# Performance work log

Hardware: AMD Instinct MI355X
Metric: run time of the kernel (lower is better)

## Reference

```python
import jax, jax.numpy as jnp
import numpy as np

BLOCKS, LAYERS, KS = 4, 2, 2
DILATIONS = [2 ** i for _ in range(BLOCKS) for i in range(LAYERS)]  # [1,2]*4
B, C_IN, N, T = 16, 2, 2048, 12
RC, DC, SC, EC, OUT = 32, 32, 256, 512, 12
L = BLOCKS * LAYERS
BN_EPS = 1e-5


def setup_inputs() -> dict:
    key = jax.random.key(0)
    ks = jax.random.split(key, 24)
    # raw inputs
    x = jax.random.normal(ks[0], (B, C_IN, N, T), dtype=jnp.float32)
    # two fixed supports: row-normalized random adjacency (dense, as in GraphWaveNet transition matrices)
    A_raw = jax.random.uniform(ks[1], (2, N, N), dtype=jnp.float32)
    A = A_raw / jnp.sum(A_raw, axis=2, keepdims=True)
    nodevec1 = jax.random.normal(ks[2], (N, 10), dtype=jnp.float32)
    nodevec2 = jax.random.normal(ks[3], (10, N), dtype=jnp.float32)
    s = 0.1  # weight scale to keep activations in a sane range
    filter_w = jax.random.normal(ks[4], (L, DC, RC, KS), dtype=jnp.float32) * s
    filter_b = jax.random.normal(ks[5], (L, DC), dtype=jnp.float32) * s
    gate_w = jax.random.normal(ks[6], (L, DC, RC, KS), dtype=jnp.float32) * s
    gate_b = jax.random.normal(ks[7], (L, DC), dtype=jnp.float32) * s
    skip_w = jax.random.normal(ks[8], (L, SC, DC), dtype=jnp.float32) * s
    skip_b = jax.random.normal(ks[9], (L, SC), dtype=jnp.float32) * s
    gcn_w = jax.random.normal(ks[10], (L, RC, 7 * DC), dtype=jnp.float32) * s
    gcn_b = jax.random.normal(ks[11], (L, RC), dtype=jnp.float32) * s
    bn_gamma = 1.0 + 0.1 * jax.random.normal(ks[12], (L, RC), dtype=jnp.float32)
    bn_beta = 0.1 * jax.random.normal(ks[13], (L, RC), dtype=jnp.float32)
    bn_mean = 0.1 * jax.random.normal(ks[14], (L, RC), dtype=jnp.float32)
    bn_var = 1.0 + jax.random.uniform(ks[15], (L, RC), dtype=jnp.float32)
    start_w = jax.random.normal(ks[16], (RC, C_IN), dtype=jnp.float32) * s
    start_b = jax.random.normal(ks[17], (RC,), dtype=jnp.float32) * s
    end1_w = jax.random.normal(ks[18], (EC, SC), dtype=jnp.float32) * s
    end1_b = jax.random.normal(ks[19], (EC,), dtype=jnp.float32) * s
    end2_w = jax.random.normal(ks[20], (OUT, EC), dtype=jnp.float32) * s
    end2_b = jax.random.normal(ks[21], (OUT,), dtype=jnp.float32) * s
    return dict(x=x, A=A, nodevec1=nodevec1, nodevec2=nodevec2,
                filter_w=filter_w, filter_b=filter_b, gate_w=gate_w, gate_b=gate_b,
                skip_w=skip_w, skip_b=skip_b, gcn_w=gcn_w, gcn_b=gcn_b,
                bn_gamma=bn_gamma, bn_beta=bn_beta, bn_mean=bn_mean, bn_var=bn_var,
                start_w=start_w, start_b=start_b, end1_w=end1_w, end1_b=end1_b,
                end2_w=end2_w, end2_b=end2_b)


def _conv1x1(x, w, b):
    # x: [b,c,n,t], w: [o,c] -> [b,o,n,t]
    return jnp.einsum('oc,bcnt->bont', w, x) + b[None, :, None, None]


def _dilated_conv2(x, w, b, d):
    # kernel (1,2) with time dilation d; out length T-d (valid conv)
    xa, xb = x[..., :-d], x[..., d:]
    y = jnp.einsum('oc,bcnt->bont', w[:, :, 0], xa) + jnp.einsum('oc,bcnt->bont', w[:, :, 1], xb)
    return y + b[None, :, None, None]


def _fwd(x, A, nodevec1, nodevec2, filter_w, filter_b, gate_w, gate_b,
         skip_w, skip_b, gcn_w, gcn_b, bn_gamma, bn_beta, bn_mean, bn_var,
         start_w, start_b, end1_w, end1_b, end2_w, end2_b):
    # pad 1 step at the start of time; T becomes 13 == receptive_field
    x = jnp.pad(x, ((0, 0), (0, 0), (0, 0), (1, 0)))
    x = x[:, :2]
    x = _conv1x1(x, start_w, start_b)  # [B,RC,N,13]
    # adaptive adjacency
    adp = jax.nn.softmax(jax.nn.relu(nodevec1 @ nodevec2), axis=1)
    supports = [A[0], A[1], adp]
    skip = None
    for i, d in enumerate(DILATIONS):
        residual = x
        filt = jnp.tanh(_dilated_conv2(residual, filter_w[i], filter_b[i], d))
        gate = jax.nn.sigmoid(_dilated_conv2(residual, gate_w[i], gate_b[i], d))
        x = filt * gate  # [B,DC,N,T-d]
        s = _conv1x1(x, skip_w[i], skip_b[i])  # [B,SC,N,T']
        skip = s if skip is None else s + skip[..., -s.shape[3]:]
        # GCN: order-2 diffusion over 3 supports, concat, 1x1 mix (dropout is identity in eval)
        outs = [x]
        for a in supports:
            x1 = jnp.einsum('bcvt,vw->bcwt', x, a)
            x2 = jnp.einsum('bcvt,vw->bcwt', x1, a)
            outs.extend([x1, x2])
        h = jnp.concatenate(outs, axis=1)  # [B,7*DC,N,T']
        x = _conv1x1(h, gcn_w[i], gcn_b[i])
        x = x + residual[..., -x.shape[3]:]
        # BatchNorm2d in eval mode (running stats)
        inv = bn_gamma[i] / jnp.sqrt(bn_var[i] + BN_EPS)
        x = (x - bn_mean[i][None, :, None, None]) * inv[None, :, None, None] + bn_beta[i][None, :, None, None]
    x = jax.nn.relu(skip)
    x = jax.nn.relu(_conv1x1(x, end1_w, end1_b))
    x = _conv1x1(x, end2_w, end2_b)  # [B,OUT,N,1]
    return x


def reference(x, A, nodevec1, nodevec2, filter_w, filter_b, gate_w, gate_b,
              skip_w, skip_b, gcn_w, gcn_b, bn_gamma, bn_beta, bn_mean, bn_var,
              start_w, start_b, end1_w, end1_b, end2_w, end2_b):
    return _fwd(x, A, nodevec1, nodevec2, filter_w, filter_b, gate_w, gate_b,
                skip_w, skip_b, gcn_w, gcn_b, bn_gamma, bn_beta, bn_mean, bn_var,
                start_w, start_b, end1_w, end1_b, end2_w, end2_b)
```

## Files before the change

### kernel.cpp

```cpp
#include <hip/hip_runtime.h>
#include <math.h>


#define NNODE 2048
#define NLAYER 8
#define SSTR ((size_t)NNODE * NNODE)

typedef unsigned short u16;
typedef unsigned int u32;
typedef __attribute__((ext_vector_type(8))) short bf16x8;
typedef __attribute__((ext_vector_type(4))) float f32x4;

__device__ __forceinline__ u16 f2bf(float f) {
    unsigned u = __builtin_bit_cast(unsigned, f);
    u += 0x7fffu + ((u >> 16) & 1u);
    return (u16)(u >> 16);
}
__device__ __forceinline__ float bf2f(u16 h) {
    unsigned u = ((unsigned)h) << 16;
    return __builtin_bit_cast(float, u);
}
__device__ __forceinline__ float bflo(u32 p) { return __builtin_bit_cast(float, p << 16); }
__device__ __forceinline__ float bfhi(u32 p) { return __builtin_bit_cast(float, p & 0xffff0000u); }
__device__ __forceinline__ u32 pack2(float a, float b) {
    return (u32)f2bf(a) | ((u32)f2bf(b) << 16);
}

__device__ __forceinline__ void gld16(const void* g, void* l) {
    __builtin_amdgcn_global_load_lds(
        (const __attribute__((address_space(1))) unsigned int*)g,
        (__attribute__((address_space(3))) unsigned int*)l, 16, 0, 0);
}

__global__ __launch_bounds__(256) void k_adp_mm(const float* __restrict__ nv1,
                                                const float* __restrict__ nv2,
                                                float* __restrict__ P) {
    int v = blockIdx.y;
    int w = blockIdx.x * 256 + threadIdx.x;
    float acc = 0.f;
#pragma unroll
    for (int k = 0; k < 10; ++k) acc += nv1[v * 10 + k] * nv2[k * NNODE + w];
    P[(size_t)v * NNODE + w] = acc;
}

__global__ __launch_bounds__(256) void k_softmax(float* __restrict__ P) {
    int v = blockIdx.x, tid = threadIdx.x;
    float* row = P + (size_t)v * NNODE;
    float m = 0.f;
    for (int w = tid; w < NNODE; w += 256) m = fmaxf(m, fmaxf(row[w], 0.f));
#pragma unroll
    for (int off = 32; off > 0; off >>= 1) m = fmaxf(m, __shfl_down(m, off));
    __shared__ float redm[4];
    __shared__ float reds[4];
    int wave = tid >> 6, lane = tid & 63;
    if (lane == 0) redm[wave] = m;
    __syncthreads();
    m = fmaxf(fmaxf(redm[0], redm[1]), fmaxf(redm[2], redm[3]));
    float s = 0.f;
    for (int w = tid; w < NNODE; w += 256) s += expf(fmaxf(row[w], 0.f) - m);
#pragma unroll
    for (int off = 32; off > 0; off >>= 1) s += __shfl_down(s, off);
    if (lane == 0) reds[wave] = s;
    __syncthreads();
    s = reds[0] + reds[1] + reds[2] + reds[3];
    float inv = 1.f / s;
    for (int w = tid; w < NNODE; w += 256) row[w] = expf(fmaxf(row[w], 0.f) - m) * inv;
}

__global__ __launch_bounds__(256) void k_transp(const float* __restrict__ A,
                                                const float* __restrict__ adp,
                                                u16* __restrict__ ST,
                                                u16* __restrict__ Sbf) {
    __shared__ float tile[32][33];
    int s = blockIdx.z;
    const float* src = (s < 2) ? (A + (size_t)s * SSTR) : adp;
    int v0 = blockIdx.y * 32, w0 = blockIdx.x * 32;
    int tx = threadIdx.x & 31, ty = threadIdx.x >> 5;
    u16* dst2 = Sbf + (size_t)s * SSTR;
#pragma unroll
    for (int p = 0; p < 4; ++p) {
        float v = src[(size_t)(v0 + ty + p * 8) * NNODE + w0 + tx];
        tile[ty + p * 8][tx] = v;
        dst2[(size_t)(v0 + ty + p * 8) * NNODE + w0 + tx] = f2bf(v);
    }
    __syncthreads();
    u16* dst = ST + (size_t)(2 * s) * SSTR;
#pragma unroll
    for (int p = 0; p < 4; ++p)
        dst[(size_t)(w0 + ty + p * 8) * NNODE + v0 + tx] = f2bf(tile[tx][ty + p * 8]);
}

__global__ __launch_bounds__(256) void k_gemm_mfma(
    const u16* __restrict__ A, int lda, size_t asstr,
    const u16* __restrict__ BT, size_t bsstr,
    u16* __restrict__ C, int ldc, size_t csstr, int sbase) {
    __shared__ u16 Asl[128 * 32];
    __shared__ u16 Bsl[128 * 32];
    const int tid = threadIdx.x;
    const int wave = tid >> 6, lane = tid & 63;
    const int sidx = sbase + blockIdx.z;
    const u16* Ab = A + sidx * asstr + (size_t)blockIdx.y * 128 * lda;
    const u16* Bb = BT + sidx * bsstr + (size_t)blockIdx.x * 128 * NNODE;
    const int tr = tid >> 2;
    const int tc = (tid & 3) * 8;
    char* AslB = (char*)Asl + wave * 1024;
    char* BslB = (char*)Bsl + wave * 1024;
    const int wm = (wave & 1) * 64, wn = (wave >> 1) * 64;
    const int fr = lane & 15;
    const int fk = (lane >> 4) * 8;
    f32x4 acc[4][4];
#pragma unroll
    for (int i = 0; i < 4; ++i)
#pragma unroll
        for (int j = 0; j < 4; ++j) acc[i][j] = (f32x4){0.f, 0.f, 0.f, 0.f};

    for (int k0 = 0; k0 < 2048; k0 += 32) {
        gld16(Ab + (size_t)tr * lda + k0 + tc, AslB);
        gld16(Ab + (size_t)(tr + 64) * lda + k0 + tc, AslB + 4096);
        gld16(Bb + (size_t)tr * NNODE + k0 + tc, BslB);
        gld16(Bb + (size_t)(tr + 64) * NNODE + k0 + tc, BslB + 4096);
        __syncthreads();
        bf16x8 af[4], bf[4];
#pragma unroll
        for (int i = 0; i < 4; ++i)
            af[i] = *(const bf16x8*)&Asl[(wm + i * 16 + fr) * 32 + fk];
#pragma unroll
        for (int j = 0; j < 4; ++j)
            bf[j] = *(const bf16x8*)&Bsl[(wn + j * 16 + fr) * 32 + fk];
#pragma unroll
        for (int i = 0; i < 4; ++i)
#pragma unroll
            for (int j = 0; j < 4; ++j)
                acc[i][j] = __builtin_amdgcn_mfma_f32_16x16x32_bf16(af[i], bf[j], acc[i][j], 0, 0, 0);
        __syncthreads();
    }
    u16* Cb = C + sidx * csstr + (size_t)(blockIdx.y * 128 + wm) * ldc + blockIdx.x * 128 + wn;
    const int orow = (lane >> 4) * 4;
#pragma unroll
    for (int i = 0; i < 4; ++i)
#pragma unroll
        for (int j = 0; j < 4; ++j)
#pragma unroll
            for (int r = 0; r < 4; ++r)
                Cb[(size_t)(i * 16 + orow + r) * ldc + j * 16 + fr] = f2bf(acc[i][j][r]);
}

__global__ __launch_bounds__(256) void k_gemmZ(const u16* __restrict__ Xg,
                                               const u16* __restrict__ ST,
                                               u16* __restrict__ Z, int pass) {
    __shared__ u16 Asl[2][128 * 32];
    __shared__ u16 Bsl[2][128 * 32];
    const int tid = threadIdx.x;
    const int wave = tid >> 6, lane = tid & 63;
    const int m0 = blockIdx.y * 128;
    const int slice = pass * 3 + (blockIdx.x >> 4);
    const int nIn = (blockIdx.x & 15) * 128;
    const u16* Ab = Xg + (size_t)m0 * 2048;
    const u16* Bb = ST + (size_t)slice * SSTR + (size_t)nIn * NNODE;
    const int tr = tid >> 2;
    const int tc = (tid & 3) * 8;
    char* AslB0 = (char*)Asl[0] + wave * 1024;
    char* AslB1 = (char*)Asl[1] + wave * 1024;
    char* BslB0 = (char*)Bsl[0] + wave * 1024;
    char* BslB1 = (char*)Bsl[1] + wave * 1024;
    const int wm = (wave & 1) * 64, wn = (wave >> 1) * 64;
    const int fr = lane & 15;
    const int fk = (lane >> 4) * 8;
    f32x4 acc[4][4];
#pragma unroll
    for (int i = 0; i < 4; ++i)
#pragma unroll
        for (int j = 0; j < 4; ++j) acc[i][j] = (f32x4){0.f, 0.f, 0.f, 0.f};

    for (int k0 = 0; k0 < 2048; k0 += 64) {
        gld16(Ab + (size_t)tr * 2048 + k0 + tc, AslB0);
        gld16(Ab + (size_t)(tr + 64) * 2048 + k0 + tc, AslB0 + 4096);
        gld16(Ab + (size_t)tr * 2048 + k0 + 32 + tc, AslB1);
        gld16(Ab + (size_t)(tr + 64) * 2048 + k0 + 32 + tc, AslB1 + 4096);
        gld16(Bb + (size_t)tr * NNODE + k0 + tc, BslB0);
        gld16(Bb + (size_t)(tr + 64) * NNODE + k0 + tc, BslB0 + 4096);
        gld16(Bb + (size_t)tr * NNODE + k0 + 32 + tc, BslB1);
        gld16(Bb + (size_t)(tr + 64) * NNODE + k0 + 32 + tc, BslB1 + 4096);
        __syncthreads();
#pragma unroll
        for (int h = 0; h < 2; ++h) {
            bf16x8 af[4], bf[4];
#pragma unroll
            for (int i = 0; i < 4; ++i)
                af[i] = *(const bf16x8*)&Asl[h][(wm + i * 16 + fr) * 32 + fk];
#pragma unroll
            for (int j = 0; j < 4; ++j)
                bf[j] = *(const bf16x8*)&Bsl[h][(wn + j * 16 + fr) * 32 + fk];
#pragma unroll
            for (int i = 0; i < 4; ++i)
#pragma unroll
                for (int j = 0; j < 4; ++j)
                    acc[i][j] = __builtin_amdgcn_mfma_f32_16x16x32_bf16(af[i], bf[j], acc[i][j], 0, 0, 0);
        }
        __syncthreads();
    }
    u16* Cb = Z + (size_t)(m0 + wm) * 6144 + blockIdx.x * 128 + wn;
    const int orow = (lane >> 4) * 4;
#pragma unroll
    for (int i = 0; i < 4; ++i)
#pragma unroll
        for (int j = 0; j < 4; ++j)
#pragma unroll
            for (int r = 0; r < 4; ++r)
                Cb[(size_t)(i * 16 + orow + r) * 6144 + j * 16 + fr] = f2bf(acc[i][j][r]);
}

__global__ __launch_bounds__(256) void k_start(const float* __restrict__ xin,
                                               const float* __restrict__ sw,
                                               const float* __restrict__ sb,
                                               u16* __restrict__ out, int b0) {
    int n = blockIdx.x * 256 + threadIdx.x;
    int t = blockIdx.y;
    int bl = blockIdx.z;
    int b = b0 + bl;
    float x0 = 0.f, x1 = 0.f;
    if (t > 0) {
        x0 = xin[((size_t)(b * 2 + 0) * NNODE + n) * 12 + (t - 1)];
        x1 = xin[((size_t)(b * 2 + 1) * NNODE + n) * 12 + (t - 1)];
    }
#pragma unroll
    for (int co = 0; co < 32; ++co) {
        float v = sw[co * 2 + 0] * x0 + sw[co * 2 + 1] * x1 + sb[co];
        out[((size_t)(bl * 32 + co) * 13 + t) * NNODE + n] = f2bf(v);
    }
}

__global__ __launch_bounds__(256) void k_gate(const u16* __restrict__ cur,
                                              u16* __restrict__ xg,
                                              u16* __restrict__ nxt,
                                              int T, int Tn, int d,
                                              const float* __restrict__ fw,
                                              const float* __restrict__ fb,
                                              const float* __restrict__ gw,
                                              const float* __restrict__ gb,
                                              const float* __restrict__ gcwl,
                                              const float* __restrict__ gcbl,
                                              int donxt) {
    __shared__ float4 wp[1024];
    __shared__ float w0[32][33];
    int tid = threadIdx.x;
#pragma unroll
    for (int u = 0; u < 4; ++u) {
        int idx = tid + u * 256;
        int ci = idx >> 5, co = idx & 31;
        wp[idx] = make_float4(fw[co * 64 + ci * 2], fw[co * 64 + ci * 2 + 1],
                              gw[co * 64 + ci * 2], gw[co * 64 + ci * 2 + 1]);
        w0[ci][co] = gcwl[co * 224 + ci];
    }
    __syncthreads();
    int n = blockIdx.x * 512 + tid * 2;
    int t = blockIdx.y;
    int bl = blockIdx.z;
    float f0[32], f1[32], g0[32], g1[32];
#pragma unroll
    for (int co = 0; co < 32; ++co) { f0[co] = 0.f; f1[co] = 0.f; g0[co] = 0.f; g1[co] = 0.f; }
    for (int ci = 0; ci < 32; ++ci) {
        size_t ba = ((size_t)(bl * 32 + ci) * T + t) * NNODE + n;
        size_t bb = ((size_t)(bl * 32 + ci) * T + t + d) * NNODE + n;
        u32 ua = *(const u32*)&cur[ba];
        u32 ub = *(const u32*)&cur[bb];
        float xa0 = bflo(ua), xa1 = bfhi(ua);
        float xb0 = bflo(ub), xb1 = bfhi(ub);
#pragma unroll
        for (int co = 0; co < 32; ++co) {
            float4 w = wp[ci * 32 + co];
            f0[co] += w.x * xa0 + w.y * xb0;
            f1[co] += w.x * xa1 + w.y * xb1;
            g0[co] += w.z * xa0 + w.w * xb0;
            g1[co] += w.z * xa1 + w.w * xb1;
        }
    }
#pragma unroll
    for (int co = 0; co < 32; ++co) {
        float fbv = fb[co], gbv = gb[co];
        float a0 = tanhf(f0[co] + fbv) * (1.f / (1.f + expf(-(g0[co] + gbv))));
        float a1 = tanhf(f1[co] + fbv) * (1.f / (1.f + expf(-(g1[co] + gbv))));
        f0[co] = a0; f1[co] = a1;
        size_t o = ((size_t)(bl * 32 + co) * Tn + t) * NNODE + n;
        *(u32*)&xg[o] = pack2(a0, a1);
    }
    if (donxt) {
#pragma unroll
        for (int cop = 0; cop < 32; ++cop) {
            float s0 = gcbl[cop], s1 = s0;
#pragma unroll
            for (int ci = 0; ci < 32; ++ci) {
                float wv = w0[ci][cop];
                s0 += wv * f0[ci];
                s1 += wv * f1[ci];
            }
            size_t o = ((size_t)(bl * 32 + cop) * Tn + t) * NNODE + n;
            *(u32*)&nxt[o] = pack2(s0, s1);
        }
    }
}

__global__ __launch_bounds__(256) void k_skip(const u16* __restrict__ xg,
                                              float* __restrict__ skip, int Tn,
                                              const float* __restrict__ sw,
                                              const float* __restrict__ sb, int b0, int init) {
    __shared__ float wl[256];
    int tid = threadIdx.x;
    int sc0 = blockIdx.y * 8;
    wl[tid] = sw[sc0 * 32 + tid];
    __syncthreads();
    int n = blockIdx.x * 512 + tid * 2;
    int bl = blockIdx.z;
    float a0[8], a1[8];
#pragma unroll
    for (int j = 0; j < 8; ++j) { a0[j] = 0.f; a1[j] = 0.f; }
    for (int ci = 0; ci < 32; ci += 2) {
        u32 p0 = *(const u32*)&xg[((size_t)(bl * 32 + ci + 0) * Tn + (Tn - 1)) * NNODE + n];
        u32 p1 = *(const u32*)&xg[((size_t)(bl * 32 + ci + 1) * Tn + (Tn - 1)) * NNODE + n];
        float v00 = bflo(p0), v01 = bfhi(p0);
        float v10 = bflo(p1), v11 = bfhi(p1);
#pragma unroll
        for (int j = 0; j < 8; ++j) {
            float wA = wl[j * 32 + ci], wB = wl[j * 32 + ci + 1];
            a0[j] += wA * v00 + wB * v10;
            a1[j] += wA * v01 + wB * v11;
        }
    }
    int b = b0 + bl;
#pragma unroll
    for (int j = 0; j < 8; ++j) {
        size_t o = ((size_t)(b * 256) + sc0 + j) * NNODE + n;
        float bsv = sb[sc0 + j];
        if (init) {
            *(float2*)&skip[o] = make_float2(a0[j] + bsv, a1[j] + bsv);
        } else {
            float2 old = *(const float2*)&skip[o];
            *(float2*)&skip[o] = make_float2(old.x + a0[j] + bsv, old.y + a1[j] + bsv);
        }
    }
}

__global__ __launch_bounds__(256) void k_accum(const u16* __restrict__ Z,
                                               int cbase,
                                               const float* __restrict__ gcnw,
                                               u16* __restrict__ outp,
                                               const u16* __restrict__ resid,
                                               int Tn, int d, int finalf,
                                               const float* __restrict__ bng,
                                               const float* __restrict__ bnb,
                                               const float* __restrict__ bnm,
                                               const float* __restrict__ bnv) {
    __shared__ float wl[3][32][32];
    int tid = threadIdx.x;
    for (int u = tid; u < 3072; u += 256) {
        int g = u >> 10, ci = (u >> 5) & 31, co = u & 31;
        wl[g][ci][co] = gcnw[co * 224 + cbase + g * 32 + ci];
    }
    __syncthreads();
    int n = blockIdx.x * 512 + tid * 2;
    int t = blockIdx.y, bl = blockIdx.z;
    float a0[32], a1[32];
#pragma unroll
    for (int co = 0; co < 32; ++co) { a0[co] = 0.f; a1[co] = 0.f; }
    for (int ci = 0; ci < 32; ++ci) {
        size_t m = (size_t)(bl * 32 + ci) * Tn + t;
#pragma unroll
        for (int g = 0; g < 3; ++g) {
            u32 zz = *(const u32*)&Z[m * 6144 + g * 2048 + n];
            float v0 = bflo(zz), v1 = bfhi(zz);
#pragma unroll
            for (int cq = 0; cq < 8; ++cq) {
                float4 w = *(const float4*)&wl[g][ci][cq * 4];
                a0[cq * 4 + 0] += w.x * v0; a1[cq * 4 + 0] += w.x * v1;
                a0[cq * 4 + 1] += w.y * v0; a1[cq * 4 + 1] += w.y * v1;
                a0[cq * 4 + 2] += w.z * v0; a1[cq * 4 + 2] += w.z * v1;
                a0[cq * 4 + 3] += w.w * v0; a1[cq * 4 + 3] += w.w * v1;
            }
        }
    }
#pragma unroll
    for (int co = 0; co < 32; ++co) {
        size_t o = ((size_t)(bl * 32 + co) * Tn + t) * NNODE + n;
        u32 oo = *(const u32*)&outp[o];
        float v0 = bflo(oo) + a0[co];
        float v1 = bfhi(oo) + a1[co];
        if (finalf) {
            size_t ro = ((size_t)(bl * 32 + co) * (Tn + d) + t + d) * NNODE + n;
            u32 rr = *(const u32*)&resid[ro];
            v0 += bflo(rr); v1 += bfhi(rr);
            float inv = bng[co] * rsqrtf(bnv[co] + 1e-5f);
            float mu = bnm[co], be = bnb[co];
            v0 = (v0 - mu) * inv + be;
            v1 = (v1 - mu) * inv + be;
        }
        *(u32*)&outp[o] = pack2(v0, v1);
    }
}

__global__ __launch_bounds__(256) void k_skipT(const float* __restrict__ skip,
                                               u16* __restrict__ skipT) {
    __shared__ float tile[32][33];
    int b = blockIdx.z;
    int n0 = blockIdx.x * 32, c0 = blockIdx.y * 32;
    int tx = threadIdx.x & 31, ty = threadIdx.x >> 5;
#pragma unroll
    for (int p = 0; p < 4; ++p)
        tile[ty + p * 8][tx] = skip[((size_t)b * 256 + c0 + ty + p * 8) * NNODE + n0 + tx];
    __syncthreads();
#pragma unroll
    for (int p = 0; p < 4; ++p)
        skipT[((size_t)b * NNODE + n0 + ty + p * 8) * 256 + c0 + tx] =
            f2bf(fmaxf(tile[tx][ty + p * 8], 0.f));
}

__global__ __launch_bounds__(256) void k_cast(const float* __restrict__ src,
                                              u16* __restrict__ dst) {
    int i = blockIdx.x * 256 + threadIdx.x;
    dst[i] = f2bf(src[i]);
}

__global__ __launch_bounds__(256) void k_end1m(const u16* __restrict__ E1,
                                               const u16* __restrict__ skT,
                                               const float* __restrict__ bias,
                                               u16* __restrict__ h) {
    __shared__ u16 Asl[128 * 32];
    __shared__ u16 Bsl[128 * 32];
    const int tid = threadIdx.x;
    const int wave = tid >> 6, lane = tid & 63;
    const int b = blockIdx.z;
    const int m0 = blockIdx.y * 128;
    const int n0 = blockIdx.x * 128;
    const int tr = tid >> 2;
    const int tc = (tid & 3) * 8;
    char* AslB = (char*)Asl + wave * 1024;
    char* BslB = (char*)Bsl + wave * 1024;
    const int wm = (wave & 1) * 64, wn = (wave >> 1) * 64;
    const int fr = lane & 15;
    const int fk = (lane >> 4) * 8;
    const u16* Ab = E1 + (size_t)m0 * 256;
    const u16* Bb = skT + ((size_t)b * NNODE + n0) * 256;
    f32x4 acc[4][4];
#pragma unroll
    for (int i = 0; i < 4; ++i)
#pragma unroll
        for (int j = 0; j < 4; ++j) acc[i][j] = (f32x4){0.f, 0.f, 0.f, 0.f};
    for (int k0 = 0; k0 < 256; k0 += 32) {
        gld16(Ab + (size_t)tr * 256 + k0 + tc, AslB);
        gld16(Ab + (size_t)(tr + 64) * 256 + k0 + tc, AslB + 4096);
        gld16(Bb + (size_t)tr * 256 + k0 + tc, BslB);
        gld16(Bb + (size_t)(tr + 64) * 256 + k0 + tc, BslB + 4096);
        __syncthreads();
        bf16x8 af[4], bf[4];
#pragma unroll
        for (int i = 0; i < 4; ++i)
            af[i] = *(const bf16x8*)&Asl[(wm + i * 16 + fr) * 32 + fk];
#pragma unroll
        for (int j = 0; j < 4; ++j)
            bf[j] = *(const bf16x8*)&Bsl[(wn + j * 16 + fr) * 32 + fk];
#pragma unroll
        for (int i = 0; i < 4; ++i)
#pragma unroll
            for (int j = 0; j < 4; ++j)
                acc[i][j] = __builtin_amdgcn_mfma_f32_16x16x32_bf16(af[i], bf[j], acc[i][j], 0, 0, 0);
        __syncthreads();
    }
    const int orow = (lane >> 4) * 4;
#pragma unroll
    for (int i = 0; i < 4; ++i)
#pragma unroll
        for (int r = 0; r < 4; ++r) {
            int m = m0 + wm + i * 16 + orow + r;
            float bs = bias[m];
            size_t ob = ((size_t)b * 512 + m) * NNODE + n0 + wn;
#pragma unroll
            for (int j = 0; j < 4; ++j)
                h[ob + j * 16 + fr] = f2bf(fmaxf(acc[i][j][r] + bs, 0.f));
        }
}

__global__ __launch_bounds__(256) void k_end2(const u16* __restrict__ h,
                                              const float* __restrict__ w,
                                              const float* __restrict__ bias,
                                              float* __restrict__ out) {
    __shared__ float wl[12][512];
    int tid = threadIdx.x;
    for (int u = tid; u < 6144; u += 256) wl[u >> 9][u & 511] = w[u];
    __syncthreads();
    int n = blockIdx.x * 256 + tid;
    int b = blockIdx.y;
    float acc[12];
#pragma unroll
    for (int o = 0; o < 12; ++o) acc[o] = 0.f;
#pragma unroll 4
    for (int e = 0; e < 512; ++e) {
        float v = bf2f(h[((size_t)(b * 512) + e) * NNODE + n]);
#pragma unroll
        for (int o = 0; o < 12; ++o) acc[o] += wl[o][e] * v;
    }
#pragma unroll
    for (int o = 0; o < 12; ++o)
        out[((size_t)(b * 12) + o) * NNODE + n] = acc[o] + bias[o];
}

extern "C" void kernel_launch(void* const* d_in, const int* in_sizes, int n_in,
                              void* d_out, int out_size, void* d_ws, size_t ws_size,
                              hipStream_t stream) {
    const float* x_in = (const float*)d_in[0];
    const float* A    = (const float*)d_in[1];
    const float* nv1  = (const float*)d_in[2];
    const float* nv2  = (const float*)d_in[3];
    const float* fw   = (const float*)d_in[4];
    const float* fb   = (const float*)d_in[5];
    const float* gw   = (const float*)d_in[6];
    const float* gb   = (const float*)d_in[7];
    const float* skw  = (const float*)d_in[8];
    const float* skb  = (const float*)d_in[9];
    const float* gcw  = (const float*)d_in[10];
    const float* gcb  = (const float*)d_in[11];
    const float* bng  = (const float*)d_in[12];
    const float* bnb  = (const float*)d_in[13];
    const float* bnm  = (const float*)d_in[14];
    const float* bnv  = (const float*)d_in[15];
    const float* stw  = (const float*)d_in[16];
    const float* stb  = (const float*)d_in[17];
    const float* e1w  = (const float*)d_in[18];
    const float* e1b  = (const float*)d_in[19];
    const float* e2w  = (const float*)d_in[20];
    const float* e2b  = (const float*)d_in[21];
    (void)in_sizes; (void)n_in; (void)out_size;

    const int BL = (ws_size >= 239075328UL) ? 16 : 8;
    const int nch = 16 / BL;
    const size_t bufsz = (size_t)BL * 1703936UL;

    char* base = (char*)d_ws;
    u16*   ST   = (u16*)base;
    float* skip = (float*)(base + 50331648UL);
    u16*   bufA = (u16*)(base + 83886080UL);
    u16*   bufB = (u16*)(base + 83886080UL + bufsz);
    u16*   xg   = (u16*)(base + 83886080UL + 2 * bufsz);
    u16*   Z    = (u16*)(base + 83886080UL + 2 * bufsz + (size_t)BL * 1572864UL);
    float* adp  = (float*)Z;
    u16*   Sbf  = (u16*)bufA;
    u16*   h     = (u16*)(base + 83886080UL);
    u16*   skipT = (u16*)(base + 83886080UL + 33554432UL);
    u16*   E1bf  = (u16*)ST;

    k_adp_mm<<<dim3(8, 2048), 256, 0, stream>>>(nv1, nv2, adp);
    k_softmax<<<2048, 256, 0, stream>>>(adp);
    k_transp<<<dim3(64, 64, 3), 256, 0, stream>>>(A, adp, ST, Sbf);
    k_gemm_mfma<<<dim3(16, 16, 3), 256, 0, stream>>>(
        ST, NNODE, 2 * SSTR, Sbf, SSTR, ST + SSTR, NNODE, 2 * SSTR, 0);

    static const int DIL[NLAYER] = {1, 2, 1, 2, 1, 2, 1, 2};
    for (int ch = 0; ch < nch; ++ch) {
        int b0 = ch * BL;
        k_start<<<dim3(8, 13, BL), 256, 0, stream>>>(x_in, stw, stb, bufA, b0);
        u16* cur = bufA;
        u16* nxt = bufB;
        int T = 13;
        for (int i = 0; i < NLAYER; ++i) {
            int d = DIL[i], Tn = T - d;
            int last = (i == NLAYER - 1);
            k_gate<<<dim3(4, Tn, BL), 256, 0, stream>>>(cur, xg, nxt, T, Tn, d,
                fw + i * 2048, fb + i * 32, gw + i * 2048, gb + i * 32,
                gcw + i * 32 * 224, gcb + i * 32, last ? 0 : 1);
            k_skip<<<dim3(4, 32, BL), 256, 0, stream>>>(xg, skip, Tn,
                skw + i * 256 * 32, skb + i * 256, b0, (i == 0) ? 1 : 0);
            if (last) break;
            int MB = BL * Tn / 4;
            const float* gcwi = gcw + i * 32 * 224;
            for (int p = 0; p < 2; ++p) {
                k_gemmZ<<<dim3(48, MB), 256, 0, stream>>>(xg, ST, Z, p);
                k_accum<<<dim3(4, Tn, BL), 256, 0, stream>>>(
                    Z, 32 + 96 * p, gcwi, nxt, cur, Tn, d, p,
                    bng + i * 32, bnb + i * 32, bnm + i * 32, bnv + i * 32);
            }
            u16* tmp = cur; cur = nxt; nxt = tmp;
            T = Tn;
        }
    }
    k_cast<<<512, 256, 0, stream>>>(e1w, E1bf);
    k_skipT<<<dim3(64, 8, 16), 256, 0, stream>>>(skip, skipT);
    k_end1m<<<dim3(16, 4, 16), 256, 0, stream>>>(E1bf, skipT, e1b, h);
    k_end2<<<dim3(8, 16), 256, 0, stream>>>(h, e2w, e2b, (float*)d_out);
}
```

Before: 3.173 ms.

## Enlarge k_gemmZ tile to 256x128 with triple-buffered LDS pipeline

Result: slower. 3.639 ms (+14.7%).

```diff
diff --git a/kernel.cpp b/kernel.cpp
--- a/kernel.cpp
+++ b/kernel.cpp
@@ -145,64 +145,116 @@
                 Cb[(size_t)(i * 16 + orow + r) * ldc + j * 16 + fr] = f2bf(acc[i][j][r]);
 }
 
+__device__ __forceinline__ void stage_call_A(const u16* Ap, int kk, int c,
+                                             char* slotb, int woff) {
+    gld16(Ap + kk + c * 131072, slotb + c * 4096 + woff);
+}
+__device__ __forceinline__ void stage_call_B(const u16* Bp, int kk, int c,
+                                             char* slotb, int woff) {
+    gld16(Bp + kk + c * 131072, slotb + 16384 + c * 4096 + woff);
+}
+
 __global__ __launch_bounds__(256) void k_gemmZ(const u16* __restrict__ Xg,
                                                const u16* __restrict__ ST,
                                                u16* __restrict__ Z, int pass) {
-    __shared__ u16 Asl[2][128 * 32];
-    __shared__ u16 Bsl[2][128 * 32];
+    __shared__ __align__(16) u16 lds[3][12288];
     const int tid = threadIdx.x;
     const int wave = tid >> 6, lane = tid & 63;
-    const int m0 = blockIdx.y * 128;
+    const int m0 = blockIdx.y * 256;
     const int slice = pass * 3 + (blockIdx.x >> 4);
     const int nIn = (blockIdx.x & 15) * 128;
     const u16* Ab = Xg + (size_t)m0 * 2048;
     const u16* Bb = ST + (size_t)slice * SSTR + (size_t)nIn * NNODE;
-    const int tr = tid >> 2;
-    const int tc = (tid & 3) * 8;
-    char* AslB0 = (char*)Asl[0] + wave * 1024;
-    char* AslB1 = (char*)Asl[1] + wave * 1024;
-    char* BslB0 = (char*)Bsl[0] + wave * 1024;
-    char* BslB1 = (char*)Bsl[1] + wave * 1024;
-    const int wm = (wave & 1) * 64, wn = (wave >> 1) * 64;
+    const int srow = wave * 16 + (lane >> 2);
+    const int scol = (lane & 3) * 8;
+    const u16* Ap = Ab + (size_t)srow * 2048 + scol;
+    const u16* Bp = Bb + (size_t)srow * 2048 + scol;
+    const int woff = wave * 1024;
+    const int wm = (wave & 1) * 128;
+    const int wn = (wave >> 1) * 64;
     const int fr = lane & 15;
     const int fk = (lane >> 4) * 8;
-    f32x4 acc[4][4];
-#pragma unroll
-    for (int i = 0; i < 4; ++i)
+
+    f32x4 acc[8][4];
+#pragma unroll
+    for (int i = 0; i < 8; ++i)
 #pragma unroll
         for (int j = 0; j < 4; ++j) acc[i][j] = (f32x4){0.f, 0.f, 0.f, 0.f};
 
-    for (int k0 = 0; k0 < 2048; k0 += 64) {
-        gld16(Ab + (size_t)tr * 2048 + k0 + tc, AslB0);
-        gld16(Ab + (size_t)(tr + 64) * 2048 + k0 + tc, AslB0 + 4096);
-        gld16(Ab + (size_t)tr * 2048 + k0 + 32 + tc, AslB1);
-        gld16(Ab + (size_t)(tr + 64) * 2048 + k0 + 32 + tc, AslB1 + 4096);
-        gld16(Bb + (size_t)tr * NNODE + k0 + tc, BslB0);
-        gld16(Bb + (size_t)(tr + 64) * NNODE + k0 + tc, BslB0 + 4096);
-        gld16(Bb + (size_t)tr * NNODE + k0 + 32 + tc, BslB1);
-        gld16(Bb + (size_t)(tr + 64) * NNODE + k0 + 32 + tc, BslB1 + 4096);
-        __syncthreads();
-#pragma unroll
-        for (int h = 0; h < 2; ++h) {
-            bf16x8 af[4], bf[4];
-#pragma unroll
-            for (int i = 0; i < 4; ++i)
-                af[i] = *(const bf16x8*)&Asl[h][(wm + i * 16 + fr) * 32 + fk];
-#pragma unroll
-            for (int j = 0; j < 4; ++j)
-                bf[j] = *(const bf16x8*)&Bsl[h][(wn + j * 16 + fr) * 32 + fk];
-#pragma unroll
-            for (int i = 0; i < 4; ++i)
-#pragma unroll
-                for (int j = 0; j < 4; ++j)
-                    acc[i][j] = __builtin_amdgcn_mfma_f32_16x16x32_bf16(af[i], bf[j], acc[i][j], 0, 0, 0);
-        }
-        __syncthreads();
-    }
+    u16* s0 = lds[0];
+    u16* s1 = lds[1];
+    u16* s2 = lds[2];
+
+    {
+        char* b0 = (char*)s0;
+        char* b1 = (char*)s1;
+        stage_call_A(Ap, 0, 0, b0, woff);
+        stage_call_A(Ap, 0, 1, b0, woff);
+        stage_call_A(Ap, 0, 2, b0, woff);
+        stage_call_A(Ap, 0, 3, b0, woff);
+        stage_call_B(Bp, 0, 0, b0, woff);
+        stage_call_B(Bp, 0, 1, b0, woff);
+        stage_call_A(Ap, 32, 0, b1, woff);
+        stage_call_A(Ap, 32, 1, b1, woff);
+        stage_call_A(Ap, 32, 2, b1, woff);
+        stage_call_A(Ap, 32, 3, b1, woff);
+        stage_call_B(Bp, 32, 0, b1, woff);
+        stage_call_B(Bp, 32, 1, b1, woff);
+    }
+    asm volatile("s_waitcnt vmcnt(6)" ::: "memory");
+    asm volatile("s_barrier" ::: "memory");
+
+    for (int kt = 0; kt < 64; ++kt) {
+        const int ks = (kt + 2) * 32;
+        const bool do_stage = (kt < 62);
+        char* s2b = (char*)s2;
+        if (do_stage) {
+            stage_call_A(Ap, ks, 0, s2b, woff);
+            stage_call_A(Ap, ks, 1, s2b, woff);
+            stage_call_A(Ap, ks, 2, s2b, woff);
+        }
+        bf16x8 af[8];
+#pragma unroll
+        for (int i = 0; i < 8; ++i)
+            af[i] = *(const bf16x8*)&s0[(wm + i * 16 + fr) * 32 + fk];
+        bf16x8 bf0 = *(const bf16x8*)&s0[8192 + (wn + 0 * 16 + fr) * 32 + fk];
+        bf16x8 bf1 = *(const bf16x8*)&s0[8192 + (wn + 1 * 16 + fr) * 32 + fk];
+        __builtin_amdgcn_s_setprio(1);
+#pragma unroll
+        for (int i = 0; i < 8; ++i)
+            acc[i][0] = __builtin_amdgcn_mfma_f32_16x16x32_bf16(af[i], bf0, acc[i][0], 0, 0, 0);
+#pragma unroll
+        for (int i = 0; i < 8; ++i)
+            acc[i][1] = __builtin_amdgcn_mfma_f32_16x16x32_bf16(af[i], bf1, acc[i][1], 0, 0, 0);
+        __builtin_amdgcn_s_setprio(0);
+        if (do_stage) {
+            stage_call_A(Ap, ks, 3, s2b, woff);
+            stage_call_B(Bp, ks, 0, s2b, woff);
+            stage_call_B(Bp, ks, 1, s2b, woff);
+        }
+        bf16x8 bf2 = *(const bf16x8*)&s0[8192 + (wn + 2 * 16 + fr) * 32 + fk];
+        bf16x8 bf3 = *(const bf16x8*)&s0[8192 + (wn + 3 * 16 + fr) * 32 + fk];
+        __builtin_amdgcn_s_setprio(1);
+#pragma unroll
+        for (int i = 0; i < 8; ++i)
+            acc[i][2] = __builtin_amdgcn_mfma_f32_16x16x32_bf16(af[i], bf2, acc[i][2], 0, 0, 0);
+#pragma unroll
+        for (int i = 0; i < 8; ++i)
+            acc[i][3] = __builtin_amdgcn_mfma_f32_16x16x32_bf16(af[i], bf3, acc[i][3], 0, 0, 0);
+        __builtin_amdgcn_s_setprio(0);
+        if (kt < 62) {
+            asm volatile("s_waitcnt vmcnt(6)" ::: "memory");
+        } else {
+            asm volatile("s_waitcnt vmcnt(0)" ::: "memory");
+        }
+        asm volatile("s_barrier" ::: "memory");
+        u16* t = s0; s0 = s1; s1 = s2; s2 = t;
+    }
+
     u16* Cb = Z + (size_t)(m0 + wm) * 6144 + blockIdx.x * 128 + wn;
     const int orow = (lane >> 4) * 4;
 #pragma unroll
-    for (int i = 0; i < 4; ++i)
+    for (int i = 0; i < 8; ++i)
 #pragma unroll
         for (int j = 0; j < 4; ++j)
 #pragma unroll
@@ -568,7 +620,7 @@
             k_skip<<<dim3(4, 32, BL), 256, 0, stream>>>(xg, skip, Tn,
                 skw + i * 256 * 32, skb + i * 256, b0, (i == 0) ? 1 : 0);
             if (last) break;
-            int MB = BL * Tn / 4;
+            int MB = BL * Tn / 8;
             const float* gcwi = gcw + i * 32 * 224;
             for (int p = 0; p < 2; ++p) {
                 k_gemmZ<<<dim3(48, MB), 256, 0, stream>>>(xg, ST, Z, p);
```

## Rewrite graph-diffusion GEMM with 256x256 tiles, swizzled LDS, and pipelined prefetch

Applied to the files above, without the earlier changes.

Result: no change. 3.134 ms (-1.2%).

```diff
diff --git a/kernel.cpp b/kernel.cpp
--- a/kernel.cpp
+++ b/kernel.cpp
@@ -145,64 +145,155 @@
                 Cb[(size_t)(i * 16 + orow + r) * ldc + j * 16 + fr] = f2bf(acc[i][j][r]);
 }
 
-__global__ __launch_bounds__(256) void k_gemmZ(const u16* __restrict__ Xg,
-                                               const u16* __restrict__ ST,
-                                               u16* __restrict__ Z, int pass) {
-    __shared__ u16 Asl[2][128 * 32];
-    __shared__ u16 Bsl[2][128 * 32];
+__global__ __launch_bounds__(512, 2) void k_gemmZ(const u16* __restrict__ Xg,
+                                                  const u16* __restrict__ ST,
+                                                  u16* __restrict__ Z, int pass) {
+    __shared__ __align__(16) char ldsb[131072];
     const int tid = threadIdx.x;
     const int wave = tid >> 6, lane = tid & 63;
-    const int m0 = blockIdx.y * 128;
-    const int slice = pass * 3 + (blockIdx.x >> 4);
-    const int nIn = (blockIdx.x & 15) * 128;
-    const u16* Ab = Xg + (size_t)m0 * 2048;
-    const u16* Bb = ST + (size_t)slice * SSTR + (size_t)nIn * NNODE;
-    const int tr = tid >> 2;
-    const int tc = (tid & 3) * 8;
-    char* AslB0 = (char*)Asl[0] + wave * 1024;
-    char* AslB1 = (char*)Asl[1] + wave * 1024;
-    char* BslB0 = (char*)Bsl[0] + wave * 1024;
-    char* BslB1 = (char*)Bsl[1] + wave * 1024;
-    const int wm = (wave & 1) * 64, wn = (wave >> 1) * 64;
+    const int m0 = blockIdx.y * 256;
+    const int slice = pass * 3 + (blockIdx.x >> 3);
+    const int n0 = (blockIdx.x & 7) * 256;
+    const u16* AbG = Xg + (size_t)m0 * 2048;
+    const u16* BbG = ST + (size_t)slice * SSTR + (size_t)n0 * 2048;
+
+    const int xorc = ((tid & 7) ^ ((tid >> 3) & 7)) << 3;
+    const size_t aRow = (size_t)(tid >> 3) * 2048 + xorc;
+    const int bRowLoc = ((tid >> 8) << 6) + (((tid >> 6) & 3) << 3) + ((tid >> 3) & 7);
+    const size_t bRow = (size_t)bRowLoc * 2048 + xorc;
+    const int aw = wave << 10;
+    const int bw = ((wave >> 2) << 13) + ((wave & 3) << 10);
+
     const int fr = lane & 15;
-    const int fk = (lane >> 4) * 8;
-    f32x4 acc[4][4];
-#pragma unroll
-    for (int i = 0; i < 4; ++i)
+    const int cl4 = lane >> 4;
+    const int ch0 = (cl4 ^ (fr & 7)) << 4;
+    const int ch1 = ch0 ^ 64;
+    const int aRd = ((wave & 1) << 14) + fr * 128;
+    const int bRd = ((wave >> 1) << 13) + fr * 128;
+    const int wm = (wave & 1) << 7;
+    const int wn = (wave >> 1) << 6;
+
+    char* A0 = ldsb;
+    char* A1 = ldsb + 32768;
+    char* B0 = ldsb + 65536;
+    char* B1 = ldsb + 98304;
+
+    auto STA = [&](char* Abase, int k0, int q) {
+        const size_t g = (size_t)(q << 6) * 2048 + aRow + k0;
+        gld16(AbG + g, Abase + (q << 13) + aw);
+        gld16(AbG + g + (size_t)128 * 2048, Abase + 16384 + (q << 13) + aw);
+    };
+    auto STB = [&](char* Bbase, int k0, int q) {
+        const size_t g = (size_t)(q << 5) * 2048 + bRow + k0;
+        gld16(BbG + g, Bbase + (q << 12) + bw);
+        gld16(BbG + g + (size_t)128 * 2048, Bbase + 16384 + (q << 12) + bw);
+    };
+
+    f32x4 acc[8][4];
+#pragma unroll
+    for (int i = 0; i < 8; ++i)
 #pragma unroll
         for (int j = 0; j < 4; ++j) acc[i][j] = (f32x4){0.f, 0.f, 0.f, 0.f};
 
-    for (int k0 = 0; k0 < 2048; k0 += 64) {
-        gld16(Ab + (size_t)tr * 2048 + k0 + tc, AslB0);
-        gld16(Ab + (size_t)(tr + 64) * 2048 + k0 + tc, AslB0 + 4096);
-        gld16(Ab + (size_t)tr * 2048 + k0 + 32 + tc, AslB1);
-        gld16(Ab + (size_t)(tr + 64) * 2048 + k0 + 32 + tc, AslB1 + 4096);
-        gld16(Bb + (size_t)tr * NNODE + k0 + tc, BslB0);
-        gld16(Bb + (size_t)(tr + 64) * NNODE + k0 + tc, BslB0 + 4096);
-        gld16(Bb + (size_t)tr * NNODE + k0 + 32 + tc, BslB1);
-        gld16(Bb + (size_t)(tr + 64) * NNODE + k0 + 32 + tc, BslB1 + 4096);
-        __syncthreads();
-#pragma unroll
-        for (int h = 0; h < 2; ++h) {
-            bf16x8 af[4], bf[4];
-#pragma unroll
-            for (int i = 0; i < 4; ++i)
-                af[i] = *(const bf16x8*)&Asl[h][(wm + i * 16 + fr) * 32 + fk];
-#pragma unroll
-            for (int j = 0; j < 4; ++j)
-                bf[j] = *(const bf16x8*)&Bsl[h][(wn + j * 16 + fr) * 32 + fk];
-#pragma unroll
-            for (int i = 0; i < 4; ++i)
-#pragma unroll
-                for (int j = 0; j < 4; ++j)
-                    acc[i][j] = __builtin_amdgcn_mfma_f32_16x16x32_bf16(af[i], bf[j], acc[i][j], 0, 0, 0);
-        }
-        __syncthreads();
-    }
-    u16* Cb = Z + (size_t)(m0 + wm) * 6144 + blockIdx.x * 128 + wn;
-    const int orow = (lane >> 4) * 4;
-#pragma unroll
-    for (int i = 0; i < 4; ++i)
+    STA(A0, 0, 0); STA(A0, 0, 1); STB(B0, 0, 0); STB(B0, 0, 1);
+    STA(A1, 64, 0); STB(B1, 64, 0); STB(B1, 64, 1);
+    asm volatile("s_waitcnt vmcnt(6)" ::: "memory");
+    asm volatile("s_barrier" ::: "memory");
+
+    char *Ac = A0, *Ao = A1, *Bc = B0, *Bo = B1;
+    bf16x8 af[4][2], bfl[2][2], bfh[2][2];
+
+    for (int T = 0; T < 32; ++T) {
+#pragma unroll
+        for (int i = 0; i < 4; ++i) {
+            af[i][0] = *(const bf16x8*)(Ac + aRd + (i << 11) + ch0);
+            af[i][1] = *(const bf16x8*)(Ac + aRd + (i << 11) + ch1);
+        }
+#pragma unroll
+        for (int j = 0; j < 2; ++j) {
+            bfl[j][0] = *(const bf16x8*)(Bc + bRd + (j << 11) + ch0);
+            bfl[j][1] = *(const bf16x8*)(Bc + bRd + (j << 11) + ch1);
+        }
+        if (T < 31) STA(Ao, (T + 1) * 64, 1);
+        asm volatile("s_barrier" ::: "memory");
+        asm volatile("s_waitcnt lgkmcnt(0)" ::: "memory");
+        __builtin_amdgcn_sched_barrier(0);
+        __builtin_amdgcn_s_setprio(1);
+#pragma unroll
+        for (int i = 0; i < 4; ++i)
+#pragma unroll
+            for (int j = 0; j < 2; ++j) {
+                acc[i][j] = __builtin_amdgcn_mfma_f32_16x16x32_bf16(af[i][0], bfl[j][0], acc[i][j], 0, 0, 0);
+                acc[i][j] = __builtin_amdgcn_mfma_f32_16x16x32_bf16(af[i][1], bfl[j][1], acc[i][j], 0, 0, 0);
+            }
+        __builtin_amdgcn_s_setprio(0);
+        asm volatile("s_barrier" ::: "memory");
+#pragma unroll
+        for (int j = 0; j < 2; ++j) {
+            bfh[j][0] = *(const bf16x8*)(Bc + bRd + 4096 + (j << 11) + ch0);
+            bfh[j][1] = *(const bf16x8*)(Bc + bRd + 4096 + (j << 11) + ch1);
+        }
+        if (T < 30) STA(Ac, (T + 2) * 64, 0);
+        asm volatile("s_barrier" ::: "memory");
+        asm volatile("s_waitcnt lgkmcnt(0)" ::: "memory");
+        __builtin_amdgcn_sched_barrier(0);
+        __builtin_amdgcn_s_setprio(1);
+#pragma unroll
+        for (int i = 0; i < 4; ++i)
+#pragma unroll
+            for (int j = 0; j < 2; ++j) {
+                acc[i][2 + j] = __builtin_amdgcn_mfma_f32_16x16x32_bf16(af[i][0], bfh[j][0], acc[i][2 + j], 0, 0, 0);
+                acc[i][2 + j] = __builtin_amdgcn_mfma_f32_16x16x32_bf16(af[i][1], bfh[j][1], acc[i][2 + j], 0, 0, 0);
+            }
+        __builtin_amdgcn_s_setprio(0);
+        asm volatile("s_barrier" ::: "memory");
+#pragma unroll
+        for (int i = 0; i < 4; ++i) {
+            af[i][0] = *(const bf16x8*)(Ac + aRd + 8192 + (i << 11) + ch0);
+            af[i][1] = *(const bf16x8*)(Ac + aRd + 8192 + (i << 11) + ch1);
+        }
+        if (T < 30) STB(Bc, (T + 2) * 64, 0);
+        asm volatile("s_barrier" ::: "memory");
+        asm volatile("s_waitcnt lgkmcnt(0)" ::: "memory");
+        __builtin_amdgcn_sched_barrier(0);
+        __builtin_amdgcn_s_setprio(1);
+#pragma unroll
+        for (int i = 0; i < 4; ++i)
+#pragma unroll
+            for (int j = 0; j < 2; ++j) {
+                acc[4 + i][2 + j] = __builtin_amdgcn_mfma_f32_16x16x32_bf16(af[i][0], bfh[j][0], acc[4 + i][2 + j], 0, 0, 0);
+                acc[4 + i][2 + j] = __builtin_amdgcn_mfma_f32_16x16x32_bf16(af[i][1], bfh[j][1], acc[4 + i][2 + j], 0, 0, 0);
+            }
+        __builtin_amdgcn_s_setprio(0);
+        asm volatile("s_barrier" ::: "memory");
+        if (T < 30) STB(Bc, (T + 2) * 64, 1);
+        asm volatile("s_barrier" ::: "memory");
+        __builtin_amdgcn_sched_barrier(0);
+        __builtin_amdgcn_s_setprio(1);
+#pragma unroll
+        for (int i = 0; i < 4; ++i)
+#pragma unroll
+            for (int j = 0; j < 2; ++j) {
+                acc[4 + i][j] = __builtin_amdgcn_mfma_f32_16x16x32_bf16(af[i][0], bfl[j][0], acc[4 + i][j], 0, 0, 0);
+                acc[4 + i][j] = __builtin_amdgcn_mfma_f32_16x16x32_bf16(af[i][1], bfl[j][1], acc[4 + i][j], 0, 0, 0);
+            }
+        __builtin_amdgcn_s_setprio(0);
+        if (T < 30) {
+            asm volatile("s_waitcnt vmcnt(6)" ::: "memory");
+        } else if (T == 30) {
+            asm volatile("s_waitcnt vmcnt(0)" ::: "memory");
+        }
+        asm volatile("s_barrier" ::: "memory");
+        char* t;
+        t = Ac; Ac = Ao; Ao = t;
+        t = Bc; Bc = Bo; Bo = t;
+    }
+
+    const int col0 = (blockIdx.x >> 3) * 2048 + (blockIdx.x & 7) * 256;
+    u16* Cb = Z + (size_t)(m0 + wm) * 6144 + col0 + wn;
+    const int orow = cl4 * 4;
+#pragma unroll
+    for (int i = 0; i < 8; ++i)
 #pragma unroll
         for (int j = 0; j < 4; ++j)
 #pragma unroll
@@ -568,10 +659,10 @@
             k_skip<<<dim3(4, 32, BL), 256, 0, stream>>>(xg, skip, Tn,
                 skw + i * 256 * 32, skb + i * 256, b0, (i == 0) ? 1 : 0);
             if (last) break;
-            int MB = BL * Tn / 4;
+            int MB = BL * Tn / 8;
             const float* gcwi = gcw + i * 32 * 224;
             for (int p = 0; p < 2; ++p) {
-                k_gemmZ<<<dim3(48, MB), 256, 0, stream>>>(xg, ST, Z, p);
+                k_gemmZ<<<dim3(24, MB), 512, 0, stream>>>(xg, ST, Z, p);
                 k_accum<<<dim3(4, Tn, BL), 256, 0, stream>>>(
                     Z, 32 + 96 * p, gcwi, nxt, cur, Tn, d, p,
                     bng + i * 32, bnb + i * 32, bnm + i * 32, bnv + i * 32);
```
